# Performance work log

Measured on AMD Instinct MI355X. Metric: run time of the kernel, lower is better.

Reference implementation:

```python
import jax, jax.numpy as jnp
import numpy as np

LN_EPS = 1e-5
DELTA_FACTOR = 0.01
PATCH_KH, PATCH_KW = 4, 4
SIGMA = 2.0


def layernorm(x, g, b):
    m = jnp.mean(x, axis=-1, keepdims=True)
    v = jnp.var(x, axis=-1, keepdims=True)
    return (x - m) * jax.lax.rsqrt(v + LN_EPS) * g + b


def grid_sample(src, grid):
    # src [B,C,H,W], grid [B,Hg,Wg,2] in [-1,1]; bilinear, align_corners=False, zero padding
    B, C, H, W = src.shape
    Hg, Wg = grid.shape[1], grid.shape[2]
    gx = (grid[..., 0] + 1.0) * (W * 0.5) - 0.5
    gy = (grid[..., 1] + 1.0) * (H * 0.5) - 0.5
    x0 = jnp.floor(gx)
    y0 = jnp.floor(gy)
    wx = gx - x0
    wy = gy - y0
    x0i = x0.astype(jnp.int32)
    y0i = y0.astype(jnp.int32)
    flat = src.reshape(B, C, H * W)

    def tap(xi, yi, w):
        valid = (xi >= 0) & (xi < W) & (yi >= 0) & (yi < H)
        idx = (jnp.clip(yi, 0, H - 1) * W + jnp.clip(xi, 0, W - 1)).reshape(B, -1)
        vals = jax.vmap(lambda f, i: f[:, i])(flat, idx)  # [B,C,Hg*Wg]
        return vals * (w * valid).reshape(B, 1, -1)

    out = (tap(x0i, y0i, (1 - wx) * (1 - wy)) + tap(x0i + 1, y0i, wx * (1 - wy))
           + tap(x0i, y0i + 1, (1 - wx) * wy) + tap(x0i + 1, y0i + 1, wx * wy))
    return out.reshape(B, C, Hg, Wg)


def gaussian_filt(x, k, sigma):
    # depthwise Gaussian blur, NCHW
    C = x.shape[1]
    coords = jnp.arange(k, dtype=x.dtype) - (k - 1) / 2.0
    g2 = jnp.exp(-(coords[:, None] ** 2 + coords[None, :] ** 2) / (2.0 * sigma ** 2))
    g2 = g2 / g2.sum()
    kern = jnp.broadcast_to(g2, (C, 1, k, k))
    p = (k - 1) // 2
    return jax.lax.conv_general_dilated(x, kern, (1, 1), [(p, p), (p, p)],
                                        dimension_numbers=('NCHW', 'OIHW', 'NCHW'),
                                        feature_group_count=C)


def reconstruct_feature(feature, mask, k, sigma):
    if k <= 1:
        return feature
    feature = feature * mask
    out = gaussian_filt(jnp.concatenate([feature, mask], axis=1), k, sigma)
    f_i = out[:, :-1]
    m_i = out[:, -1:]
    f_i = f_i / (m_i + 1e-6)
    f_i = f_i * (m_i > 0)
    return feature + (1 - mask) * f_i


def token2map(x, loc, H, W, k, sigma):
    B, N, C = x.shape
    l = jnp.clip(loc, 0.0, 1.0) * jnp.array([W - 1, H - 1], dtype=loc.dtype)
    l = jnp.round(l).astype(jnp.int32)
    idx = l[..., 0] + l[..., 1] * W + (jnp.arange(B, dtype=jnp.int32) * (H * W))[:, None]
    vals = jnp.concatenate([x, jnp.ones((B, N, 1), x.dtype)], axis=-1).reshape(B * N, C + 1)
    out = jnp.zeros((B * H * W, C + 1), x.dtype).at[idx.reshape(-1)].add(vals)
    out = out.reshape(B, H, W, C + 1).transpose(0, 3, 1, 2)
    feat, mask = out[:, :-1], out[:, -1:]
    feat = feat / (mask + 1e-6)
    mask = (mask > 0).astype(x.dtype)
    feat = feat * mask
    return reconstruct_feature(feat, mask, k, sigma)


def forward(x, loc, src, H, W, kernel_size,
            w_delta, b_delta, norm1_g, norm1_b, conv_w, conv_b,
            norm2_g, norm2_b, fc1_w, fc1_b, fc2_w, fc2_b):
    B, N, _ = loc.shape
    Cs, Hs, Ws = src.shape[1], src.shape[2], src.shape[3]
    delta = (layernorm(x, norm1_g, norm1_b) @ w_delta + b_delta) * DELTA_FACTOR
    loc_extra = jnp.clip(loc + delta, 0.0, 1.0)
    # extract_local_feature: 4x4 sub-pixel patch around each extra location
    xo = (jnp.arange(PATCH_KW, dtype=loc.dtype) - (PATCH_KW - 1) / 2.0) / (Ws - 1)
    yo = (jnp.arange(PATCH_KH, dtype=loc.dtype) - (PATCH_KH - 1) / 2.0) / (Hs - 1)
    off = jnp.stack([jnp.broadcast_to(xo[None, :], (PATCH_KH, PATCH_KW)),
                     jnp.broadcast_to(yo[:, None], (PATCH_KH, PATCH_KW))], axis=-1)
    grid = (loc_extra[:, :, None, None, :] + off[None, None]) * 2.0 - 1.0  # [B,N,kh,kw,2]
    patches = grid_sample(src, grid.reshape(B, N, PATCH_KH * PATCH_KW, 2))  # [B,C,N,kh*kw]
    patches = patches.reshape(B, Cs, N, PATCH_KH, PATCH_KW)
    # local_conv: 4x4 conv stride 4 over a 4x4 patch == single dot product
    extra = jnp.einsum('bcnhw,ochw->bno', patches, conv_w) + conv_b
    extra = layernorm(extra, norm2_g, norm2_b)
    # token2map scatter + gaussian reconstruction, then gather back at loc_extra
    fmap = token2map(x, loc, H, W, kernel_size, SIGMA)
    extra_inter = grid_sample(fmap, (loc_extra * 2.0 - 1.0)[:, None, :, :])  # [B,C,1,N]
    extra_inter = extra_inter[:, :, 0].transpose(0, 2, 1)  # [B,N,C]
    extra = jnp.concatenate([extra_inter, extra], axis=-1)
    h = jax.nn.gelu(extra @ fc1_w + fc1_b, approximate=False)
    extra = h @ fc2_w + fc2_b
    return jnp.concatenate([x, extra], axis=1), jnp.concatenate([loc, loc_extra], axis=1)


def setup_inputs() -> dict:
    key = jax.random.key(0)
    ks = jax.random.split(key, 12)
    B, N, D = 4, 16384, 256
    LD, HID = 64, 4 * D
    inp = {
        'x': jax.random.normal(ks[0], (B, N, D), jnp.float32),
        'loc': jax.random.uniform(ks[1], (B, N, 2), jnp.float32),
        'src': jax.random.normal(ks[2], (B, 3, 512, 512), jnp.float32),
        'pos_embed': jnp.zeros((1,), jnp.float32),
        'H': 128, 'W': 128, 'kernel_size': 3,
        'w_delta': jax.random.normal(ks[3], (D, 2), jnp.float32) * 0.02,
        'b_delta': jnp.zeros((2,), jnp.float32),
        'norm1_g': jnp.ones((D,), jnp.float32),
        'norm1_b': jnp.zeros((D,), jnp.float32),
        'conv_w': jax.random.normal(ks[4], (LD, 3, 4, 4), jnp.float32) * 0.1,
        'conv_b': jnp.zeros((LD,), jnp.float32),
        'norm2_g': jnp.ones((LD,), jnp.float32),
        'norm2_b': jnp.zeros((LD,), jnp.float32),
        'fc1_w': jax.random.normal(ks[5], (D + LD, HID), jnp.float32) * 0.02,
        'fc1_b': jnp.zeros((HID,), jnp.float32),
        'fc2_w': jax.random.normal(ks[6], (HID, D), jnp.float32) * 0.02,
        'fc2_b': jnp.zeros((D,), jnp.float32),
    }
    return inp


def reference(x, loc, src, pos_embed, H, W, kernel_size,
              w_delta, b_delta, norm1_g, norm1_b, conv_w, conv_b,
              norm2_g, norm2_b, fc1_w, fc1_b, fc2_w, fc2_b):
    # pos_embed is accepted by the torch forward but never used
    return forward(x, loc, src, H, W, kernel_size,
                   w_delta, b_delta, norm1_g, norm1_b, conv_w, conv_b,
                   norm2_g, norm2_b, fc1_w, fc1_b, fc2_w, fc2_b)
```

## Files before the change

### kernel.cpp

```cpp
#include <hip/hip_runtime.h>
#include <hip/hip_bf16.h>

#define B_    4
#define N_    16384
#define D_    256
#define LD_   64
#define HID_  1024
#define HW_   128
#define HSRC_ 512
#define CS_   3
#define KIN_  320

typedef __attribute__((ext_vector_type(8))) short bf16x8;
typedef __attribute__((ext_vector_type(4))) float f32x4;

__device__ __forceinline__ float wsum(float v) {
#pragma unroll
  for (int off = 32; off; off >>= 1) v += __shfl_xor(v, off, 64);
  return v;
}

__device__ __forceinline__ unsigned short f2bf(float f) {
  unsigned int u = __float_as_uint(f);
  u = (u + 0x7fffu + ((u >> 16) & 1u)) >> 16;
  return (unsigned short)u;
}
__device__ __forceinline__ float b2f(unsigned short u) {
  return __uint_as_float(((unsigned int)u) << 16);
}

__device__ __forceinline__ float gelu_f(float x) {
  float z = 0.7978845608028654f * (x + 0.044715f * x * x * x);
  float e = __expf(2.0f * z);
  float th = 1.0f - 2.0f / (e + 1.0f);
  return 0.5f * x * (1.0f + th);
}

__device__ __forceinline__ void async16(unsigned short* lds, const unsigned short* g) {
  __builtin_amdgcn_global_load_lds(
      (const __attribute__((address_space(1))) unsigned int*)g,
      (__attribute__((address_space(3))) unsigned int*)lds, 16, 0, 0);
}

__global__ __launch_bounds__(256) void k_wconv(const float* __restrict__ fc1w,
                                               const float* __restrict__ fc2w,
                                               unsigned short* __restrict__ bt1,
                                               unsigned short* __restrict__ bt2) {
  int i = blockIdx.x * 256 + threadIdx.x;
  if (i < KIN_ * HID_) {
    int n = i / KIN_, k = i % KIN_;
    bt1[i] = f2bf(fc1w[(size_t)k * HID_ + n]);
  } else {
    int j = i - KIN_ * HID_;
    if (j < D_ * HID_) {
      int n = j / HID_, k = j % HID_;
      bt2[j] = f2bf(fc2w[(size_t)k * D_ + n]);
    }
  }
}

__global__ __launch_bounds__(256) void k_delta(const float* __restrict__ x,
                                               const float* __restrict__ loc,
                                               const float* __restrict__ wd,
                                               const float* __restrict__ bd,
                                               const float* __restrict__ g1,
                                               const float* __restrict__ b1,
                                               float* __restrict__ locex,
                                               float* __restrict__ out1,
                                               float* __restrict__ out0,
                                               int* __restrict__ head,
                                               int* __restrict__ nxt) {
  int wv = threadIdx.x >> 6, lane = threadIdx.x & 63;
  int t = blockIdx.x * 4 + wv;
  int b = t >> 14, n = t & (N_ - 1);
  const float4 xv = *(const float4*)(x + (size_t)t * D_ + lane * 4);
  *(float4*)(out0 + ((size_t)b * 2 * N_ + n) * D_ + lane * 4) = xv;
  float m = wsum(xv.x + xv.y + xv.z + xv.w) * (1.0f / D_);
  float d0 = xv.x - m, d1 = xv.y - m, d2 = xv.z - m, d3 = xv.w - m;
  float v = wsum(d0 * d0 + d1 * d1 + d2 * d2 + d3 * d3) * (1.0f / D_);
  float r = rsqrtf(v + 1e-5f);
  const float4 gv = *(const float4*)(g1 + lane * 4);
  const float4 bv = *(const float4*)(b1 + lane * 4);
  float n0 = d0 * r * gv.x + bv.x;
  float n1 = d1 * r * gv.y + bv.y;
  float n2 = d2 * r * gv.z + bv.z;
  float n3 = d3 * r * gv.w + bv.w;
  int i2 = lane * 8;
  float p0 = n0 * wd[i2 + 0] + n1 * wd[i2 + 2] + n2 * wd[i2 + 4] + n3 * wd[i2 + 6];
  float p1 = n0 * wd[i2 + 1] + n1 * wd[i2 + 3] + n2 * wd[i2 + 5] + n3 * wd[i2 + 7];
  p0 = wsum(p0);
  p1 = wsum(p1);
  if (lane == 0) {
    float lx = loc[(size_t)t * 2], ly = loc[(size_t)t * 2 + 1];
    float ex = fminf(fmaxf(lx + (p0 + bd[0]) * 0.01f, 0.0f), 1.0f);
    float ey = fminf(fmaxf(ly + (p1 + bd[1]) * 0.01f, 0.0f), 1.0f);
    locex[(size_t)t * 2] = ex;
    locex[(size_t)t * 2 + 1] = ey;
    size_t o1 = (size_t)b * 2 * N_;
    out1[(o1 + n) * 2 + 0] = lx;
    out1[(o1 + n) * 2 + 1] = ly;
    out1[(o1 + N_ + n) * 2 + 0] = ex;
    out1[(o1 + N_ + n) * 2 + 1] = ey;
    float cx = fminf(fmaxf(lx, 0.0f), 1.0f) * 127.0f;
    float cy = fminf(fmaxf(ly, 0.0f), 1.0f) * 127.0f;
    int ix = (int)rintf(cx);
    int iy = (int)rintf(cy);
    int cell = (b << 14) + iy * HW_ + ix;
    nxt[t] = atomicExch(head + cell, t);
  }
}

__global__ __launch_bounds__(256) void k_gather(const float* __restrict__ x,
                                                const int* __restrict__ head,
                                                const int* __restrict__ nxt,
                                                unsigned short* __restrict__ featn,
                                                float* __restrict__ cntf) {
  int cell = blockIdx.x;
  int tid = threadIdx.x;
  __shared__ int toks[16];
  __shared__ int scount, snext;
  float acc = 0.0f;
  int total = 0;
  int cur = head[cell];
  while (cur >= 0) {
    if (tid == 0) {
      int c = 0, p = cur;
      while (p >= 0 && c < 16) {
        toks[c++] = p;
        p = nxt[p];
      }
      scount = c;
      snext = p;
    }
    __syncthreads();
    int c = scount;
    for (int i = 0; i < c; ++i) acc += x[(size_t)toks[i] * D_ + tid];
    total += c;
    cur = snext;
    __syncthreads();
  }
  featn[(size_t)cell * D_ + tid] = f2bf((total > 0) ? acc / ((float)total + 1e-6f) : 0.0f);
  if (tid == 0) cntf[cell] = (float)total;
}

__global__ __launch_bounds__(256) void k_filter(const unsigned short* __restrict__ featn,
                                                const float* __restrict__ cntf,
                                                unsigned short* __restrict__ fmap) {
  int pix = blockIdx.x;
  int c = threadIdx.x;
  int b = pix >> 14;
  int p = pix & 16383;
  int y = p >> 7, xc = p & 127;
  float cc = cntf[pix];
  unsigned short outv;
  if (cc > 0.0f) {
    outv = featn[(size_t)pix * D_ + c];
  } else {
    float e1 = expf(-0.125f), e2 = expf(-0.25f);
    float sumw = 1.0f + 4.0f * e1 + 4.0f * e2;
    float gf = 0.0f, gm = 0.0f;
#pragma unroll
    for (int dy = -1; dy <= 1; ++dy)
#pragma unroll
      for (int dx = -1; dx <= 1; ++dx) {
        int ny = y + dy, nx = xc + dx;
        if (ny < 0 || ny >= HW_ || nx < 0 || nx >= HW_) continue;
        int q = (b << 14) + ny * HW_ + nx;
        if (cntf[q] > 0.0f) {
          int dd = dy * dy + dx * dx;
          float w = (dd == 0 ? 1.0f : (dd == 1 ? e1 : e2)) / sumw;
          gf += w * b2f(featn[(size_t)q * D_ + c]);
          gm += w;
        }
      }
    outv = f2bf((gm > 0.0f) ? gf / (gm + 1e-6f) : 0.0f);
  }
  fmap[(size_t)pix * D_ + c] = outv;
}

__global__ __launch_bounds__(256) void k_patch(const float* __restrict__ src,
                                               const float* __restrict__ locex,
                                               const float* __restrict__ convw,
                                               const float* __restrict__ convb,
                                               const float* __restrict__ g2,
                                               const float* __restrict__ b2,
                                               unsigned short* __restrict__ ecat) {
  __shared__ float cw[LD_ * 49];
  __shared__ float patch[4][48];
  for (int i = threadIdx.x; i < LD_ * 48; i += 256)
    cw[(i / 48) * 49 + (i % 48)] = convw[i];
  int wv = threadIdx.x >> 6, lane = threadIdx.x & 63;
  int t = blockIdx.x * 4 + wv;
  int b = t >> 14;
  float ex = locex[(size_t)t * 2], ey = locex[(size_t)t * 2 + 1];
  __syncthreads();
  if (lane < 48) {
    int c = lane >> 4, p = lane & 15, py = p >> 2, px = p & 3;
    float u = ex + ((float)px - 1.5f) / 511.0f;
    float vv = ey + ((float)py - 1.5f) / 511.0f;
    float gx = u * 512.0f - 0.5f;
    float gy = vv * 512.0f - 0.5f;
    float fx = floorf(gx), fy = floorf(gy);
    float wx = gx - fx, wy = gy - fy;
    int x0 = (int)fx, y0 = (int)fy;
    const float* plane = src + (size_t)(b * CS_ + c) * (HSRC_ * HSRC_);
    float acc = 0.0f;
#pragma unroll
    for (int ty = 0; ty < 2; ++ty)
#pragma unroll
      for (int tx = 0; tx < 2; ++tx) {
        int xi = x0 + tx, yi = y0 + ty;
        float w = (tx ? wx : 1.0f - wx) * (ty ? wy : 1.0f - wy);
        if (xi >= 0 && xi < HSRC_ && yi >= 0 && yi < HSRC_)
          acc += w * plane[yi * HSRC_ + xi];
      }
    patch[wv][lane] = acc;
  }
  __syncthreads();
  float e = convb[lane];
#pragma unroll
  for (int i = 0; i < 48; ++i) e += patch[wv][i] * cw[lane * 49 + i];
  float m = wsum(e) * (1.0f / 64.0f);
  float d = e - m;
  float v = wsum(d * d) * (1.0f / 64.0f);
  float val = d * rsqrtf(v + 1e-5f) * g2[lane] + b2[lane];
  ecat[(size_t)t * KIN_ + D_ + lane] = f2bf(val);
}

__global__ __launch_bounds__(256) void k_sample(const unsigned short* __restrict__ fmap,
                                                const float* __restrict__ locex,
                                                unsigned short* __restrict__ ecat) {
  int wv = threadIdx.x >> 6, lane = threadIdx.x & 63;
  int t = blockIdx.x * 4 + wv;
  int b = t >> 14;
  float gx = locex[(size_t)t * 2] * 128.0f - 0.5f;
  float gy = locex[(size_t)t * 2 + 1] * 128.0f - 0.5f;
  float fx = floorf(gx), fy = floorf(gy);
  float wx = gx - fx, wy = gy - fy;
  int x0 = (int)fx, y0 = (int)fy;
  const unsigned short* base = fmap + (((size_t)b << 14)) * D_;
  float4 acc = {0.0f, 0.0f, 0.0f, 0.0f};
#pragma unroll
  for (int ty = 0; ty < 2; ++ty)
#pragma unroll
    for (int tx = 0; tx < 2; ++tx) {
      int xi = x0 + tx, yi = y0 + ty;
      float w = (tx ? wx : 1.0f - wx) * (ty ? wy : 1.0f - wy);
      if (xi >= 0 && xi < HW_ && yi >= 0 && yi < HW_) {
        ushort4 f = *(const ushort4*)(base + (size_t)(yi * HW_ + xi) * D_ + lane * 4);
        acc.x += w * b2f(f.x);
        acc.y += w * b2f(f.y);
        acc.z += w * b2f(f.z);
        acc.w += w * b2f(f.w);
      }
    }
  ushort4 o;
  o.x = f2bf(acc.x);
  o.y = f2bf(acc.y);
  o.z = f2bf(acc.z);
  o.w = f2bf(acc.w);
  *(ushort4*)(ecat + (size_t)t * KIN_ + lane * 4) = o;
}

template <int GELU>
__global__ __launch_bounds__(256) void k_gemm128(const unsigned short* __restrict__ A,
                                                 const unsigned short* __restrict__ Bt,
                                                 const float* __restrict__ bias, int K,
                                                 int Nn, unsigned short* __restrict__ hout,
                                                 float* __restrict__ out0) {
  __shared__ __align__(16) unsigned short sh[32768];
  int tid = threadIdx.x, wv = tid >> 6, lane = tid & 63;
  int wm = wv & 1, wn = wv >> 1;

  int nt_cnt = gridDim.x;
  int lin = blockIdx.y * nt_cnt + blockIdx.x;
  int xcd = lin & 7;
  int slot = lin >> 3;
  int tile_n = (slot % nt_cnt) * 128;
  int tile_m = ((slot / nt_cnt) * 8 + xcd) * 128;

  f32x4 acc[4][4];
#pragma unroll
  for (int i = 0; i < 4; ++i)
#pragma unroll
    for (int j = 0; j < 4; ++j) acc[i][j] = (f32x4){0.0f, 0.0f, 0.0f, 0.0f};

  int srow = tid >> 3;
  int schunk = (tid & 7) ^ (srow & 7);
  const unsigned short* ga = A + (size_t)(tile_m + srow) * K + schunk * 8;
  const unsigned short* gb = Bt + (size_t)(tile_n + srow) * K + schunk * 8;
  size_t skip = (size_t)32 * K;
  int lofs = tid * 8;

  int ar = wm * 64 + (lane & 15);
  int br = wn * 64 + (lane & 15);
  int ksel = lane >> 4;
  int sw = lane & 7;

  int nk = K >> 6;

#pragma unroll
  for (int c = 0; c < 4; ++c) async16(sh + c * 2048 + lofs, ga + c * skip);
#pragma unroll
  for (int c = 0; c < 4; ++c) async16(sh + 8192 + c * 2048 + lofs, gb + c * skip);
  ga += 64;
  gb += 64;

  int cur = 0;
  for (int k0 = 0; k0 < nk; ++k0) {
    __builtin_amdgcn_sched_barrier(0);
    if (k0 + 1 < nk) {
      unsigned short* nb = sh + (cur ^ 16384);
#pragma unroll
      for (int c = 0; c < 4; ++c) async16(nb + c * 2048 + lofs, ga + c * skip);
#pragma unroll
      for (int c = 0; c < 4; ++c) async16(nb + 8192 + c * 2048 + lofs, gb + c * skip);
      ga += 64;
      gb += 64;
      asm volatile("s_waitcnt vmcnt(8)" ::: "memory");
    } else {
      asm volatile("s_waitcnt vmcnt(0)" ::: "memory");
    }
    __builtin_amdgcn_s_barrier();
    __builtin_amdgcn_sched_barrier(0);

    const unsigned short* As = sh + cur;
    const unsigned short* Bs = As + 8192;
#pragma unroll
    for (int j = 0; j < 2; ++j) {
      bf16x8 afr[4], bfr[4];
      int ca = ((j * 4 + ksel) ^ sw) * 8;
#pragma unroll
      for (int i = 0; i < 4; ++i) {
        afr[i] = *(const bf16x8*)(As + (ar + i * 16) * 64 + ca);
        bfr[i] = *(const bf16x8*)(Bs + (br + i * 16) * 64 + ca);
      }
#pragma unroll
      for (int mt = 0; mt < 4; ++mt)
#pragma unroll
        for (int nt = 0; nt < 4; ++nt)
          acc[mt][nt] =
              __builtin_amdgcn_mfma_f32_16x16x32_bf16(afr[mt], bfr[nt], acc[mt][nt], 0, 0, 0);
    }
    __builtin_amdgcn_sched_barrier(0);
    __builtin_amdgcn_s_barrier();
    cur ^= 16384;
  }
  __builtin_amdgcn_sched_barrier(0);

  if (GELU) {
#pragma unroll
    for (int nt = 0; nt < 4; ++nt) {
      int nl = wn * 64 + nt * 16 + (lane & 15);
      float bv = bias[tile_n + nl];
#pragma unroll
      for (int mt = 0; mt < 4; ++mt) {
        int ml = wm * 64 + mt * 16 + (lane >> 4) * 4;
#pragma unroll
        for (int r = 0; r < 4; ++r)
          sh[(ml + r) * 128 + nl] = f2bf(gelu_f(acc[mt][nt][r] + bv));
      }
    }
    __syncthreads();
#pragma unroll
    for (int it = 0; it < 8; ++it) {
      int idx = it * 256 + tid;
      int row = idx >> 4, ch = (idx & 15) * 8;
      *(uint4*)(hout + (size_t)(tile_m + row) * Nn + tile_n + ch) =
          *(const uint4*)(sh + row * 128 + ch);
    }
  } else {
#pragma unroll
    for (int nt = 0; nt < 4; ++nt) {
      int n = tile_n + wn * 64 + nt * 16 + (lane & 15);
      float bv = bias[n];
#pragma unroll
      for (int mt = 0; mt < 4; ++mt) {
        int mbase = tile_m + wm * 64 + mt * 16 + (lane >> 4) * 4;
#pragma unroll
        for (int r = 0; r < 4; ++r) {
          int m = mbase + r;
          float v = acc[mt][nt][r] + bv;
          int bb = m >> 14, ntok = m & (N_ - 1);
          out0[((size_t)bb * 2 * N_ + N_ + ntok) * D_ + n] = v;
        }
      }
    }
  }
}

extern "C" void kernel_launch(void* const* d_in, const int* in_sizes, int n_in,
                              void* d_out, int out_size, void* d_ws, size_t ws_size,
                              hipStream_t stream) {
  const float* x = (const float*)d_in[0];
  const float* loc = (const float*)d_in[1];
  const float* src = (const float*)d_in[2];
  const float* wd = (const float*)d_in[7];
  const float* bd = (const float*)d_in[8];
  const float* g1 = (const float*)d_in[9];
  const float* b1 = (const float*)d_in[10];
  const float* cw = (const float*)d_in[11];
  const float* cb = (const float*)d_in[12];
  const float* g2 = (const float*)d_in[13];
  const float* b2 = (const float*)d_in[14];
  const float* fc1w = (const float*)d_in[15];
  const float* fc1b = (const float*)d_in[16];
  const float* fc2w = (const float*)d_in[17];
  const float* fc2b = (const float*)d_in[18];

  float* out0 = (float*)d_out;
  float* out1 = out0 + (size_t)B_ * 2 * N_ * D_;

  char* ws = (char*)d_ws;
  unsigned short* featn = (unsigned short*)(ws + 0);
  unsigned short* fmap = (unsigned short*)(ws + 33554432);
  unsigned short* h = (unsigned short*)(ws + 0);
  unsigned short* ecat = (unsigned short*)(ws + 134217728);
  unsigned short* bt1 = (unsigned short*)(ws + 176160768);
  unsigned short* bt2 = (unsigned short*)(ws + 176816128);
  float* cntf = (float*)(ws + 177340416);
  float* locex = (float*)(ws + 177602560);
  int* head = (int*)(ws + 178126848);
  int* nxt = (int*)(ws + 178388992);

  hipMemsetAsync(head, 0xFF, (size_t)262144, stream);

  k_wconv<<<2304, 256, 0, stream>>>(fc1w, fc2w, bt1, bt2);
  k_delta<<<16384, 256, 0, stream>>>(x, loc, wd, bd, g1, b1, locex, out1, out0, head, nxt);
  k_gather<<<65536, 256, 0, stream>>>(x, head, nxt, featn, cntf);
  k_filter<<<65536, 256, 0, stream>>>(featn, cntf, fmap);
  k_patch<<<16384, 256, 0, stream>>>(src, locex, cw, cb, g2, b2, ecat);
  k_sample<<<16384, 256, 0, stream>>>(fmap, locex, ecat);
  k_gemm128<1><<<dim3(8, 512), 256, 0, stream>>>(ecat, bt1, fc1b, KIN_, HID_, h, nullptr);
  k_gemm128<0><<<dim3(2, 512), 256, 0, stream>>>(h, bt2, fc2b, HID_, D_, nullptr, out0);
}
```

Before: 544.0 us.

## Fuse fc1+GELU and fc2 into one MLP kernel keeping hidden in LDS

```diff
diff --git a/kernel.cpp b/kernel.cpp
--- a/kernel.cpp
+++ b/kernel.cpp
@@ -262,128 +262,139 @@
   *(ushort4*)(ecat + (size_t)t * KIN_ + lane * 4) = o;
 }
 
-template <int GELU>
-__global__ __launch_bounds__(256) void k_gemm128(const unsigned short* __restrict__ A,
-                                                 const unsigned short* __restrict__ Bt,
-                                                 const float* __restrict__ bias, int K,
-                                                 int Nn, unsigned short* __restrict__ hout,
-                                                 float* __restrict__ out0) {
-  __shared__ __align__(16) unsigned short sh[32768];
+__global__ __launch_bounds__(256, 2) void k_mlp(const unsigned short* __restrict__ ecat,
+                                                const unsigned short* __restrict__ bt1,
+                                                const unsigned short* __restrict__ bt2,
+                                                const float* __restrict__ fc1b,
+                                                const float* __restrict__ fc2b,
+                                                float* __restrict__ out0) {
+  __shared__ __align__(16) unsigned short sh[24576];
   int tid = threadIdx.x, wv = tid >> 6, lane = tid & 63;
-  int wm = wv & 1, wn = wv >> 1;
-
-  int nt_cnt = gridDim.x;
-  int lin = blockIdx.y * nt_cnt + blockIdx.x;
-  int xcd = lin & 7;
-  int slot = lin >> 3;
-  int tile_n = (slot % nt_cnt) * 128;
-  int tile_m = ((slot / nt_cnt) * 8 + xcd) * 128;
-
-  f32x4 acc[4][4];
+  int hi = lane >> 4, lo = lane & 15, sw = lane & 7;
+
+  int tile_m = blockIdx.x * 64;
+
+  bf16x8 a[10];
+  {
+    const unsigned short* arow = ecat + (size_t)(tile_m + wv * 16 + lo) * KIN_ + hi * 8;
+#pragma unroll
+    for (int kk = 0; kk < 10; ++kk) a[kk] = *(const bf16x8*)(arow + kk * 32);
+  }
+
+  f32x4 acc2[4][4];
 #pragma unroll
   for (int i = 0; i < 4; ++i)
 #pragma unroll
-    for (int j = 0; j < 4; ++j) acc[i][j] = (f32x4){0.0f, 0.0f, 0.0f, 0.0f};
-
-  int srow = tid >> 3;
-  int schunk = (tid & 7) ^ (srow & 7);
-  const unsigned short* ga = A + (size_t)(tile_m + srow) * K + schunk * 8;
-  const unsigned short* gb = Bt + (size_t)(tile_n + srow) * K + schunk * 8;
-  size_t skip = (size_t)32 * K;
-  int lofs = tid * 8;
-
-  int ar = wm * 64 + (lane & 15);
-  int br = wn * 64 + (lane & 15);
-  int ksel = lane >> 4;
-  int sw = lane & 7;
-
-  int nk = K >> 6;
-
-#pragma unroll
-  for (int c = 0; c < 4; ++c) async16(sh + c * 2048 + lofs, ga + c * skip);
-#pragma unroll
-  for (int c = 0; c < 4; ++c) async16(sh + 8192 + c * 2048 + lofs, gb + c * skip);
-  ga += 64;
-  gb += 64;
-
+    for (int j = 0; j < 4; ++j) acc2[i][j] = (f32x4){0.0f, 0.0f, 0.0f, 0.0f};
+
+#pragma unroll
+  for (int c = 0; c < 4; ++c) {
+    int L = c * 256 + tid;
+    int line = L >> 3, u = (L & 7) ^ (line & 7);
+    async16(sh + L * 8, bt1 + (size_t)line * KIN_ + u * 8);
+  }
+  int pt = 0, pk = 1;
   int cur = 0;
-  for (int k0 = 0; k0 < nk; ++k0) {
-    __builtin_amdgcn_sched_barrier(0);
-    if (k0 + 1 < nk) {
-      unsigned short* nb = sh + (cur ^ 16384);
-#pragma unroll
-      for (int c = 0; c < 4; ++c) async16(nb + c * 2048 + lofs, ga + c * skip);
-#pragma unroll
-      for (int c = 0; c < 4; ++c) async16(nb + 8192 + c * 2048 + lofs, gb + c * skip);
-      ga += 64;
-      gb += 64;
-      asm volatile("s_waitcnt vmcnt(8)" ::: "memory");
-    } else {
-      asm volatile("s_waitcnt vmcnt(0)" ::: "memory");
-    }
+
+  for (int t = 0; t < 8; ++t) {
+    f32x4 acc1[8];
+#pragma unroll
+    for (int i = 0; i < 8; ++i) acc1[i] = (f32x4){0.0f, 0.0f, 0.0f, 0.0f};
+
+#pragma unroll
+    for (int k0 = 0; k0 < 5; ++k0) {
+      __builtin_amdgcn_sched_barrier(0);
+      if (!(t == 7 && k0 == 4)) {
+        unsigned short* nb = sh + (cur ^ 8192);
+        const unsigned short* gB = bt1 + (size_t)(pt * 128) * KIN_ + pk * 64;
+#pragma unroll
+        for (int c = 0; c < 4; ++c) {
+          int L = c * 256 + tid;
+          int line = L >> 3, u = (L & 7) ^ (line & 7);
+          async16(nb + L * 8, gB + (size_t)line * KIN_ + u * 8);
+        }
+        if (++pk == 5) { pk = 0; ++pt; }
+        asm volatile("s_waitcnt vmcnt(4)" ::: "memory");
+      } else {
+        asm volatile("s_waitcnt vmcnt(0)" ::: "memory");
+      }
+      __builtin_amdgcn_s_barrier();
+      __builtin_amdgcn_sched_barrier(0);
+
+      const unsigned short* Bs = sh + cur;
+#pragma unroll
+      for (int j = 0; j < 2; ++j) {
+        bf16x8 bfr[8];
+        int ca = ((j * 4 + hi) ^ sw) * 8;
+#pragma unroll
+        for (int nt = 0; nt < 8; ++nt)
+          bfr[nt] = *(const bf16x8*)(Bs + (nt * 16 + lo) * 64 + ca);
+        __builtin_amdgcn_s_setprio(1);
+#pragma unroll
+        for (int nt = 0; nt < 8; ++nt)
+          acc1[nt] = __builtin_amdgcn_mfma_f32_16x16x32_bf16(a[k0 * 2 + j], bfr[nt],
+                                                             acc1[nt], 0, 0, 0);
+        __builtin_amdgcn_s_setprio(0);
+      }
+      __builtin_amdgcn_sched_barrier(0);
+      __builtin_amdgcn_s_barrier();
+      cur ^= 8192;
+    }
+
+    unsigned short* hb = sh + 16384;
+#pragma unroll
+    for (int nt = 0; nt < 8; ++nt) {
+      int col = nt * 16 + lo;
+      float bv = fc1b[t * 128 + col];
+      int g = col >> 3;
+#pragma unroll
+      for (int r = 0; r < 4; ++r) {
+        int m = wv * 16 + hi * 4 + r;
+        int slot = g ^ (m & 7);
+        hb[m * 128 + slot * 8 + (col & 7)] = f2bf(gelu_f(acc1[nt][r] + bv));
+      }
+    }
+    asm volatile("s_waitcnt lgkmcnt(0)" ::: "memory");
     __builtin_amdgcn_s_barrier();
     __builtin_amdgcn_sched_barrier(0);
 
-    const unsigned short* As = sh + cur;
-    const unsigned short* Bs = As + 8192;
-#pragma unroll
-    for (int j = 0; j < 2; ++j) {
-      bf16x8 afr[4], bfr[4];
-      int ca = ((j * 4 + ksel) ^ sw) * 8;
-#pragma unroll
-      for (int i = 0; i < 4; ++i) {
-        afr[i] = *(const bf16x8*)(As + (ar + i * 16) * 64 + ca);
-        bfr[i] = *(const bf16x8*)(Bs + (br + i * 16) * 64 + ca);
-      }
+#pragma unroll
+    for (int s = 0; s < 4; ++s) {
+      bf16x8 a2[4], b2[4];
+#pragma unroll
+      for (int mt = 0; mt < 4; ++mt) {
+        int row = mt * 16 + lo;
+        int slot = (s * 4 + hi) ^ (row & 7);
+        a2[mt] = *(const bf16x8*)(hb + row * 128 + slot * 8);
+      }
+#pragma unroll
+      for (int nt2 = 0; nt2 < 4; ++nt2) {
+        int n2 = wv * 64 + nt2 * 16 + lo;
+        b2[nt2] = *(const bf16x8*)(bt2 + (size_t)n2 * HID_ + t * 128 + s * 32 + hi * 8);
+      }
+      __builtin_amdgcn_s_setprio(1);
 #pragma unroll
       for (int mt = 0; mt < 4; ++mt)
 #pragma unroll
-        for (int nt = 0; nt < 4; ++nt)
-          acc[mt][nt] =
-              __builtin_amdgcn_mfma_f32_16x16x32_bf16(afr[mt], bfr[nt], acc[mt][nt], 0, 0, 0);
+        for (int nt2 = 0; nt2 < 4; ++nt2)
+          acc2[mt][nt2] = __builtin_amdgcn_mfma_f32_16x16x32_bf16(a2[mt], b2[nt2],
+                                                                  acc2[mt][nt2], 0, 0, 0);
+      __builtin_amdgcn_s_setprio(0);
     }
     __builtin_amdgcn_sched_barrier(0);
-    __builtin_amdgcn_s_barrier();
-    cur ^= 16384;
-  }
-  __builtin_amdgcn_sched_barrier(0);
-
-  if (GELU) {
-#pragma unroll
-    for (int nt = 0; nt < 4; ++nt) {
-      int nl = wn * 64 + nt * 16 + (lane & 15);
-      float bv = bias[tile_n + nl];
-#pragma unroll
-      for (int mt = 0; mt < 4; ++mt) {
-        int ml = wm * 64 + mt * 16 + (lane >> 4) * 4;
-#pragma unroll
-        for (int r = 0; r < 4; ++r)
-          sh[(ml + r) * 128 + nl] = f2bf(gelu_f(acc[mt][nt][r] + bv));
-      }
-    }
-    __syncthreads();
-#pragma unroll
-    for (int it = 0; it < 8; ++it) {
-      int idx = it * 256 + tid;
-      int row = idx >> 4, ch = (idx & 15) * 8;
-      *(uint4*)(hout + (size_t)(tile_m + row) * Nn + tile_n + ch) =
-          *(const uint4*)(sh + row * 128 + ch);
-    }
-  } else {
-#pragma unroll
-    for (int nt = 0; nt < 4; ++nt) {
-      int n = tile_n + wn * 64 + nt * 16 + (lane & 15);
-      float bv = bias[n];
-#pragma unroll
-      for (int mt = 0; mt < 4; ++mt) {
-        int mbase = tile_m + wm * 64 + mt * 16 + (lane >> 4) * 4;
-#pragma unroll
-        for (int r = 0; r < 4; ++r) {
-          int m = mbase + r;
-          float v = acc[mt][nt][r] + bv;
-          int bb = m >> 14, ntok = m & (N_ - 1);
-          out0[((size_t)bb * 2 * N_ + N_ + ntok) * D_ + n] = v;
-        }
+  }
+
+#pragma unroll
+  for (int nt2 = 0; nt2 < 4; ++nt2) {
+    int col = wv * 64 + nt2 * 16 + lo;
+    float bv = fc2b[col];
+#pragma unroll
+    for (int mt = 0; mt < 4; ++mt) {
+#pragma unroll
+      for (int r = 0; r < 4; ++r) {
+        int m = tile_m + mt * 16 + hi * 4 + r;
+        int bb = m >> 14, ntok = m & (N_ - 1);
+        out0[((size_t)bb * 2 * N_ + N_ + ntok) * D_ + col] = acc2[mt][nt2][r] + bv;
       }
     }
   }
@@ -414,7 +425,6 @@
   char* ws = (char*)d_ws;
   unsigned short* featn = (unsigned short*)(ws + 0);
   unsigned short* fmap = (unsigned short*)(ws + 33554432);
-  unsigned short* h = (unsigned short*)(ws + 0);
   unsigned short* ecat = (unsigned short*)(ws + 134217728);
   unsigned short* bt1 = (unsigned short*)(ws + 176160768);
   unsigned short* bt2 = (unsigned short*)(ws + 176816128);
@@ -431,6 +441,5 @@
   k_filter<<<65536, 256, 0, stream>>>(featn, cntf, fmap);
   k_patch<<<16384, 256, 0, stream>>>(src, locex, cw, cb, g2, b2, ecat);
   k_sample<<<16384, 256, 0, stream>>>(fmap, locex, ecat);
-  k_gemm128<1><<<dim3(8, 512), 256, 0, stream>>>(ecat, bt1, fc1b, KIN_, HID_, h, nullptr);
-  k_gemm128<0><<<dim3(2, 512), 256, 0, stream>>>(h, bt2, fc2b, HID_, D_, nullptr, out0);
-}
+  k_mlp<<<1024, 256, 0, stream>>>(ecat, bt1, bt2, fc1b, fc2b, out0);
+}
```

Result: no change. 551.3 us (+1.3%).
